# Kernel optimization log

Hardware: AMD Instinct MI355X
Metric: run time of the kernel (lower is better)

The kernel has to match this reference:

```python
import jax, jax.numpy as jnp
import numpy as np

P = 512       # protein_dim
D = 512       # drug_dim
N = 2000      # neighbors per layer
E = 300000    # binding edges per layer
ND = 100000   # total drugs
BASELINE = 6.0
LN_EPS = 1e-5


def setup_inputs() -> dict:
    key = jax.random.key(0)
    ks = jax.random.split(key, 24)
    inp = {
        "target_features": jax.random.normal(ks[0], (P,), jnp.float32),
        "form_features": jax.random.normal(ks[1], (N, P), jnp.float32),
        "role_features": jax.random.normal(ks[2], (N, P), jnp.float32),
        "form_neighbors": jnp.arange(N, dtype=jnp.int64) if jax.config.jax_enable_x64 else jnp.arange(N, dtype=jnp.int32),
        "role_neighbors": jnp.arange(N, dtype=jnp.int32),
        "form_binds_ei": jax.random.randint(ks[3], (2, E), 0, N, jnp.int32),
        "form_binds_y": jax.random.uniform(ks[4], (E,), jnp.float32) * 8.0 + 2.0,
        "role_binds_ei": jax.random.randint(ks[5], (2, E), 0, N, jnp.int32),
        "role_binds_y": jax.random.uniform(ks[6], (E,), jnp.float32) * 8.0 + 2.0,
        "drug_features": jax.random.normal(ks[7], (ND, D), jnp.float32),
    }
    inp["form_neighbors"] = jnp.arange(N, dtype=jnp.int32)
    attn_in = P * 2 + 16
    s1 = 1.0 / np.sqrt(attn_in)
    s2 = 1.0 / np.sqrt(64)
    sd = 1.0 / np.sqrt(D)
    sp = 1.0 / np.sqrt(P)
    inp["layer_emb"] = jax.random.normal(ks[8], (2, 16), jnp.float32)
    inp["W1"] = jax.random.uniform(ks[9], (attn_in, 64), jnp.float32, -s1, s1)
    inp["b1"] = jax.random.uniform(ks[10], (64,), jnp.float32, -s1, s1)
    inp["W2"] = jax.random.uniform(ks[11], (64, 1), jnp.float32, -s2, s2)
    inp["b2"] = jax.random.uniform(ks[12], (1,), jnp.float32, -s2, s2)
    inp["Wi1"] = jax.random.uniform(ks[13], (D, P), jnp.float32, -sd, sd)
    inp["bi1"] = jax.random.uniform(ks[14], (P,), jnp.float32, -sd, sd)
    inp["prelu_alpha"] = jnp.array(0.25, jnp.float32)
    inp["Wi2"] = jax.random.uniform(ks[15], (P, P), jnp.float32, -sp, sp)
    inp["bi2"] = jax.random.uniform(ks[16], (P,), jnp.float32, -sp, sp)
    inp["ln_gamma"] = jnp.ones((P,), jnp.float32)
    inp["ln_beta"] = jnp.zeros((P,), jnp.float32)
    return inp


def _pref_vectors(neighbor_ids, ei, y, drug_features):
    # Vectorized form of the per-neighbor masked gather-sum:
    # for each edge, find its neighbor slot (neighbor_ids is sorted);
    # edges whose src id is not a neighbor get zero weight.
    n = neighbor_ids.shape[0]
    pos = jnp.clip(jnp.searchsorted(neighbor_ids, ei[0]), 0, n - 1)
    valid = neighbor_ids[pos] == ei[0]
    w = jnp.where(valid, y - BASELINE, 0.0)              # [E]
    contrib = drug_features[ei[1]] * w[:, None]          # [E, D] gather (memory-bound)
    return jax.ops.segment_sum(contrib, pos, num_segments=n)  # [N, D]


def _attention(z_target, z_neighbors, l_vec, W1, b1, W2, b2):
    n = z_neighbors.shape[0]
    inp = jnp.concatenate(
        [jnp.broadcast_to(z_target, (n, z_target.shape[0])),
         z_neighbors,
         jnp.broadcast_to(l_vec, (n, l_vec.shape[0]))], axis=-1)  # [N, 2P+16]
    h = inp @ W1 + b1
    h = jnp.where(h > 0, h, 0.2 * h)  # LeakyReLU(0.2)
    return h @ W2 + b2                # [N, 1]


def reference(target_features, form_features, role_features, form_neighbors,
              role_neighbors, form_binds_ei, form_binds_y, role_binds_ei,
              role_binds_y, drug_features, layer_emb, W1, b1, W2, b2,
              Wi1, bi1, prelu_alpha, Wi2, bi2, ln_gamma, ln_beta):
    form_msgs = _pref_vectors(form_neighbors, form_binds_ei, form_binds_y, drug_features)
    role_msgs = _pref_vectors(role_neighbors, role_binds_ei, role_binds_y, drug_features)

    form_attn = _attention(target_features, form_features, layer_emb[0], W1, b1, W2, b2)
    role_attn = _attention(target_features, role_features, layer_emb[1], W1, b1, W2, b2)

    all_msgs = jnp.concatenate([form_msgs, role_msgs], axis=0)   # [2N, D]
    all_attn = jnp.concatenate([form_attn, role_attn], axis=0)   # [2N, 1]
    attn_weights = jax.nn.softmax(all_attn, axis=0)
    v_prior = jnp.sum(attn_weights * all_msgs, axis=0)           # [D]

    h = v_prior @ Wi1 + bi1
    h = jnp.where(h > 0, h, prelu_alpha * h)  # PReLU
    v = h @ Wi2 + bi2                          # [P]

    x = target_features + v
    mu = jnp.mean(x)
    var = jnp.mean(jnp.square(x - mu))
    z_refined = (x - mu) / jnp.sqrt(var + LN_EPS) * ln_gamma + ln_beta
    return (z_refined, form_msgs, role_msgs)
```

## Files before the change

### kernel.cpp

```cpp
#include <hip/hip_runtime.h>
#include <math.h>

static constexpr int PD = 512;
static constexpr float BASEV = 6.0f;
static constexpr int CAP = 320;

__global__ __launch_bounds__(256) void front_kernel(
    const int* __restrict__ ei_f, const float* __restrict__ y_f,
    const int* __restrict__ ei_r, const float* __restrict__ y_r,
    const int* __restrict__ nb_f, const int* __restrict__ nb_r,
    const float* __restrict__ target, const float* __restrict__ formF,
    const float* __restrict__ roleF, const float* __restrict__ lemb,
    const float* __restrict__ W1, const float* __restrict__ b1,
    const float* __restrict__ W2, const float* __restrict__ b2,
    int N, int E, int AB, int EBf,
    int* __restrict__ cnt, int2* __restrict__ bins,
    float* __restrict__ logits) {
    __shared__ int snb[2048];
    int b = blockIdx.x;
    if (b >= AB) {
        int b2 = b - AB;
        bool role = b2 >= EBf;
        const int* nb = role ? nb_r : nb_f;
        const int* ei = role ? ei_r : ei_f;
        const float* yy = role ? y_r : y_f;
        bool lds_ok = (N <= 2048);
        if (lds_ok) {
            for (int i = threadIdx.x; i < N; i += 256) snb[i] = nb[i];
            __syncthreads();
        }
        int base = (role ? b2 - EBf : b2) * 1024;
        int K = 32 - __clz(N);
        int v[4], lo[4], hi[4], e[4];
#pragma unroll
        for (int r = 0; r < 4; r++) {
            e[r] = base + threadIdx.x + r * 256;
            bool a = e[r] < E;
            v[r] = a ? ei[e[r]] : 0;
            lo[r] = 0; hi[r] = a ? N : 0;
        }
        if (lds_ok) {
            for (int it = 0; it < K; it++) {
#pragma unroll
                for (int r = 0; r < 4; r++) {
                    if (lo[r] < hi[r]) {
                        int mid = (lo[r] + hi[r]) >> 1;
                        if (snb[mid] < v[r]) lo[r] = mid + 1; else hi[r] = mid;
                    }
                }
            }
        } else {
            for (int it = 0; it < K; it++) {
#pragma unroll
                for (int r = 0; r < 4; r++) {
                    if (lo[r] < hi[r]) {
                        int mid = (lo[r] + hi[r]) >> 1;
                        if (nb[mid] < v[r]) lo[r] = mid + 1; else hi[r] = mid;
                    }
                }
            }
        }
#pragma unroll
        for (int r = 0; r < 4; r++) {
            if (e[r] >= E) continue;
            int pos = lo[r] < N ? lo[r] : N - 1;
            int nbp = lds_ok ? snb[pos] : nb[pos];
            if (nbp != v[r]) continue;
            int s = role ? N + pos : pos;
            float w = yy[e[r]] - BASEV;
            int slot = atomicAdd(&cnt[s], 1);
            if (slot < CAP) bins[(size_t)s * CAP + slot] = make_int2(ei[E + e[r]], __float_as_int(w));
        }
    } else {
        float* spart = (float*)snb;
        float* sc0 = spart + 256;
        float* sc1 = spart + 320;
        int jj = threadIdx.x & 63, ck = threadIdx.x >> 6;
        const float* Wc = W1 + jj;
        float tp = 0.f;
        int p0 = ck * 128;
        for (int p = p0; p < p0 + 128; p += 4) {
            float4 tv = *(const float4*)(target + p);
            tp += tv.x * Wc[(size_t)(p + 0) * 64] + tv.y * Wc[(size_t)(p + 1) * 64]
                + tv.z * Wc[(size_t)(p + 2) * 64] + tv.w * Wc[(size_t)(p + 3) * 64];
        }
        spart[ck * 64 + jj] = tp;
        __syncthreads();
        if (ck == 0) {
            float c = b1[jj] + spart[jj] + spart[64 + jj] + spart[128 + jj] + spart[192 + jj];
            float c0 = c, c1 = c;
            for (int q = 0; q < 16; q++) {
                float wq = Wc[(size_t)(2 * PD + q) * 64];
                c0 += lemb[q] * wq;
                c1 += lemb[16 + q] * wq;
            }
            sc0[jj] = c0; sc1[jj] = c1;
        }
        __syncthreads();
        int wave = threadIdx.x >> 6, lane = threadIdx.x & 63;
        int rr = b * 4 + wave;
        int nseg = 2 * N;
        if (rr >= nseg) return;
        bool rl = rr >= N;
        const float* z = rl ? roleF + (size_t)(rr - N) * PD : formF + (size_t)rr * PD;
        const float* Wz = W1 + (size_t)PD * 64 + lane;
        float hA = rl ? sc1[lane] : sc0[lane];
        float hB = 0.f, hC = 0.f, hD = 0.f;
        for (int p = 0; p < PD; p += 8) {
            float4 z0 = *(const float4*)(z + p);
            float4 z1 = *(const float4*)(z + p + 4);
            hA += z0.x * Wz[(size_t)(p + 0) * 64] + z0.y * Wz[(size_t)(p + 1) * 64];
            hB += z0.z * Wz[(size_t)(p + 2) * 64] + z0.w * Wz[(size_t)(p + 3) * 64];
            hC += z1.x * Wz[(size_t)(p + 4) * 64] + z1.y * Wz[(size_t)(p + 5) * 64];
            hD += z1.z * Wz[(size_t)(p + 6) * 64] + z1.w * Wz[(size_t)(p + 7) * 64];
        }
        float hh = (hA + hB) + (hC + hD);
        hh = hh > 0.f ? hh : 0.2f * hh;
        float vv = hh * W2[lane];
#pragma unroll
        for (int off = 32; off > 0; off >>= 1) vv += __shfl_down(vv, off, 64);
        if (lane == 0) logits[rr] = vv + b2[0];
    }
}

__global__ __launch_bounds__(128) void accum_kernel(const int* __restrict__ cnt,
                                                    const int2* __restrict__ bins,
                                                    const float* __restrict__ drug,
                                                    float* __restrict__ msgs) {
    int b = blockIdx.x;
    int t = threadIdx.x;
    int n = cnt[b]; n = n < CAP ? n : CAP;
    const int2* bb = bins + (size_t)b * CAP;
    float4 acc = make_float4(0.f, 0.f, 0.f, 0.f);
    int k = 0;
    for (; k + 7 < n; k += 8) {
        int2 e0 = bb[k + 0], e1 = bb[k + 1], e2 = bb[k + 2], e3 = bb[k + 3];
        int2 e4 = bb[k + 4], e5 = bb[k + 5], e6 = bb[k + 6], e7 = bb[k + 7];
        float4 d0 = ((const float4*)(drug + (size_t)e0.x * PD))[t];
        float4 d1 = ((const float4*)(drug + (size_t)e1.x * PD))[t];
        float4 d2 = ((const float4*)(drug + (size_t)e2.x * PD))[t];
        float4 d3 = ((const float4*)(drug + (size_t)e3.x * PD))[t];
        float4 d4 = ((const float4*)(drug + (size_t)e4.x * PD))[t];
        float4 d5 = ((const float4*)(drug + (size_t)e5.x * PD))[t];
        float4 d6 = ((const float4*)(drug + (size_t)e6.x * PD))[t];
        float4 d7 = ((const float4*)(drug + (size_t)e7.x * PD))[t];
        float w0 = __int_as_float(e0.y), w1 = __int_as_float(e1.y);
        float w2 = __int_as_float(e2.y), w3 = __int_as_float(e3.y);
        float w4 = __int_as_float(e4.y), w5 = __int_as_float(e5.y);
        float w6 = __int_as_float(e6.y), w7 = __int_as_float(e7.y);
        acc.x += w0 * d0.x; acc.y += w0 * d0.y; acc.z += w0 * d0.z; acc.w += w0 * d0.w;
        acc.x += w1 * d1.x; acc.y += w1 * d1.y; acc.z += w1 * d1.z; acc.w += w1 * d1.w;
        acc.x += w2 * d2.x; acc.y += w2 * d2.y; acc.z += w2 * d2.z; acc.w += w2 * d2.w;
        acc.x += w3 * d3.x; acc.y += w3 * d3.y; acc.z += w3 * d3.z; acc.w += w3 * d3.w;
        acc.x += w4 * d4.x; acc.y += w4 * d4.y; acc.z += w4 * d4.z; acc.w += w4 * d4.w;
        acc.x += w5 * d5.x; acc.y += w5 * d5.y; acc.z += w5 * d5.z; acc.w += w5 * d5.w;
        acc.x += w6 * d6.x; acc.y += w6 * d6.y; acc.z += w6 * d6.z; acc.w += w6 * d6.w;
        acc.x += w7 * d7.x; acc.y += w7 * d7.y; acc.z += w7 * d7.z; acc.w += w7 * d7.w;
    }
    for (; k < n; k++) {
        int2 e0 = bb[k];
        float w0 = __int_as_float(e0.y);
        float4 d0 = ((const float4*)(drug + (size_t)e0.x * PD))[t];
        acc.x += w0 * d0.x; acc.y += w0 * d0.y; acc.z += w0 * d0.z; acc.w += w0 * d0.w;
    }
    ((float4*)(msgs + (size_t)b * PD))[t] = acc;
}

__global__ __launch_bounds__(128) void vprior_kernel(const float* __restrict__ logits,
                                                     const float* __restrict__ msgs,
                                                     int nseg, float* __restrict__ v_prior) {
    __shared__ float red[128];
    int t = threadIdx.x;
    float m = -1e30f;
    for (int s = t; s < nseg; s += 128) m = fmaxf(m, logits[s]);
    red[t] = m; __syncthreads();
    for (int o = 64; o > 0; o >>= 1) { if (t < o) red[t] = fmaxf(red[t], red[t + o]); __syncthreads(); }
    m = red[0]; __syncthreads();
    float sum = 0.f;
    for (int s = t; s < nseg; s += 128) sum += expf(logits[s] - m);
    red[t] = sum; __syncthreads();
    for (int o = 64; o > 0; o >>= 1) { if (t < o) red[t] += red[t + o]; __syncthreads(); }
    float inv = 1.f / red[0];

    float4 acc = make_float4(0.f, 0.f, 0.f, 0.f);
    for (int s = blockIdx.x; s < nseg; s += gridDim.x) {
        float w = expf(logits[s] - m) * inv;
        float4 d = ((const float4*)(msgs + (size_t)s * PD))[t];
        acc.x += w * d.x; acc.y += w * d.y; acc.z += w * d.z; acc.w += w * d.w;
    }
    atomicAdd(&v_prior[4 * t + 0], acc.x);
    atomicAdd(&v_prior[4 * t + 1], acc.y);
    atomicAdd(&v_prior[4 * t + 2], acc.z);
    atomicAdd(&v_prior[4 * t + 3], acc.w);
}

__global__ __launch_bounds__(256) void mv1_kernel(const float* __restrict__ v_prior,
                                                  const float* __restrict__ Wi1,
                                                  float* __restrict__ h) {
    int b = blockIdx.x;
    int t = threadIdx.x;
    float2 acc = make_float2(0.f, 0.f);
    int d0 = b * 16;
    for (int d = d0; d < d0 + 16; d++) {
        float vd = v_prior[d];
        float2 w = ((const float2*)(Wi1 + (size_t)d * PD))[t];
        acc.x += vd * w.x; acc.y += vd * w.y;
    }
    atomicAdd(&h[2 * t + 0], acc.x);
    atomicAdd(&h[2 * t + 1], acc.y);
}

__global__ __launch_bounds__(256) void mv2_kernel(const float* __restrict__ h,
                                                  const float* __restrict__ bi1,
                                                  const float* __restrict__ alpha_p,
                                                  const float* __restrict__ Wi2,
                                                  float* __restrict__ v) {
    int b = blockIdx.x;
    int t = threadIdx.x;
    float alpha = alpha_p[0];
    float2 acc = make_float2(0.f, 0.f);
    int q0 = b * 16;
    for (int q = q0; q < q0 + 16; q++) {
        float hq = h[q] + bi1[q];
        hq = hq > 0.f ? hq : alpha * hq;
        float2 w = ((const float2*)(Wi2 + (size_t)q * PD))[t];
        acc.x += hq * w.x; acc.y += hq * w.y;
    }
    atomicAdd(&v[2 * t + 0], acc.x);
    atomicAdd(&v[2 * t + 1], acc.y);
}

__global__ __launch_bounds__(512) void final_kernel(const float* __restrict__ target,
                                                    const float* __restrict__ v,
                                                    const float* __restrict__ bi2,
                                                    const float* __restrict__ gamma,
                                                    const float* __restrict__ beta,
                                                    float* __restrict__ out) {
    __shared__ float red[512];
    int t = threadIdx.x;
    float x = target[t] + v[t] + bi2[t];
    red[t] = x; __syncthreads();
    for (int o = 256; o > 0; o >>= 1) { if (t < o) red[t] += red[t + o]; __syncthreads(); }
    float mu = red[0] * (1.f / 512.f);
    __syncthreads();
    float dx = x - mu;
    red[t] = dx * dx; __syncthreads();
    for (int o = 256; o > 0; o >>= 1) { if (t < o) red[t] += red[t + o]; __syncthreads(); }
    float var = red[0] * (1.f / 512.f);
    out[t] = dx * (1.f / sqrtf(var + 1e-5f)) * gamma[t] + beta[t];
}

extern "C" void kernel_launch(void* const* d_in, const int* in_sizes, int n_in,
                              void* d_out, int out_size, void* d_ws, size_t ws_size,
                              hipStream_t stream) {
    const float* target = (const float*)d_in[0];
    const float* formF  = (const float*)d_in[1];
    const float* roleF  = (const float*)d_in[2];
    const int*   nb_f   = (const int*)d_in[3];
    const int*   nb_r   = (const int*)d_in[4];
    const int*   ei_f   = (const int*)d_in[5];
    const float* y_f    = (const float*)d_in[6];
    const int*   ei_r   = (const int*)d_in[7];
    const float* y_r    = (const float*)d_in[8];
    const float* drug   = (const float*)d_in[9];
    const float* lemb   = (const float*)d_in[10];
    const float* W1     = (const float*)d_in[11];
    const float* b1     = (const float*)d_in[12];
    const float* W2     = (const float*)d_in[13];
    const float* b2     = (const float*)d_in[14];
    const float* Wi1    = (const float*)d_in[15];
    const float* bi1    = (const float*)d_in[16];
    const float* alpha  = (const float*)d_in[17];
    const float* Wi2    = (const float*)d_in[18];
    const float* bi2    = (const float*)d_in[19];
    const float* gamma  = (const float*)d_in[20];
    const float* beta   = (const float*)d_in[21];

    int N = in_sizes[3];
    int E = in_sizes[5] / 2;
    int nseg = 2 * N;

    int* ws = (int*)d_ws;
    int*   cnt     = ws + 0;
    float* v_prior = (float*)(ws + 4096);
    float* hbuf    = (float*)(ws + 4608);
    float* vbuf    = (float*)(ws + 5120);
    float* logits  = (float*)(ws + 5632);
    int2*  bins    = (int2*)(ws + 9728);

    float* out  = (float*)d_out;
    float* msgs = out + PD;

    hipMemsetAsync(ws, 0, 5632 * sizeof(int), stream);

    int AB  = (nseg + 3) / 4;
    int EBf = (E + 1023) / 1024;
    front_kernel<<<AB + 2 * EBf, 256, 0, stream>>>(ei_f, y_f, ei_r, y_r, nb_f, nb_r,
                                                   target, formF, roleF, lemb,
                                                   W1, b1, W2, b2, N, E, AB, EBf,
                                                   cnt, bins, logits);
    accum_kernel<<<nseg, 128, 0, stream>>>(cnt, bins, drug, msgs);
    vprior_kernel<<<64, 128, 0, stream>>>(logits, msgs, nseg, v_prior);
    mv1_kernel<<<32, 256, 0, stream>>>(v_prior, Wi1, hbuf);
    mv2_kernel<<<32, 256, 0, stream>>>(hbuf, bi1, alpha, Wi2, vbuf);
    final_kernel<<<1, 512, 0, stream>>>(target, vbuf, bi2, gamma, beta, out);
}
```

Baseline: 452.8 us.

## Use direct-index neighbor lookup, move softmax stats into accum, nontemporal bins

Result: faster. 443.3 us (-2.1%).

```diff
diff --git a/kernel.cpp b/kernel.cpp
--- a/kernel.cpp
+++ b/kernel.cpp
@@ -4,6 +4,10 @@
 static constexpr int PD = 512;
 static constexpr float BASEV = 6.0f;
 static constexpr int CAP = 320;
+
+typedef float f4v __attribute__((ext_vector_type(4)));
+typedef int   i4v __attribute__((ext_vector_type(4)));
+typedef int   i2v __attribute__((ext_vector_type(2)));
 
 __global__ __launch_bounds__(256) void front_kernel(
     const int* __restrict__ ei_f, const float* __restrict__ y_f,
@@ -16,7 +20,7 @@
     int N, int E, int AB, int EBf,
     int* __restrict__ cnt, int2* __restrict__ bins,
     float* __restrict__ logits) {
-    __shared__ int snb[2048];
+    __shared__ float sred[384];
     int b = blockIdx.x;
     if (b >= AB) {
         int b2 = b - AB;
@@ -24,55 +28,33 @@
         const int* nb = role ? nb_r : nb_f;
         const int* ei = role ? ei_r : ei_f;
         const float* yy = role ? y_r : y_f;
-        bool lds_ok = (N <= 2048);
-        if (lds_ok) {
-            for (int i = threadIdx.x; i < N; i += 256) snb[i] = nb[i];
-            __syncthreads();
-        }
         int base = (role ? b2 - EBf : b2) * 1024;
-        int K = 32 - __clz(N);
-        int v[4], lo[4], hi[4], e[4];
+        int nb0 = nb[0];
 #pragma unroll
         for (int r = 0; r < 4; r++) {
-            e[r] = base + threadIdx.x + r * 256;
-            bool a = e[r] < E;
-            v[r] = a ? ei[e[r]] : 0;
-            lo[r] = 0; hi[r] = a ? N : 0;
-        }
-        if (lds_ok) {
-            for (int it = 0; it < K; it++) {
-#pragma unroll
-                for (int r = 0; r < 4; r++) {
-                    if (lo[r] < hi[r]) {
-                        int mid = (lo[r] + hi[r]) >> 1;
-                        if (snb[mid] < v[r]) lo[r] = mid + 1; else hi[r] = mid;
-                    }
-                }
+            int e = base + threadIdx.x + r * 256;
+            if (e >= E) continue;
+            int v = ei[e];
+            int g = v - nb0; g = g < 0 ? 0 : (g >= N ? N - 1 : g);
+            int pos;
+            if (nb[g] == v && (g == 0 || nb[g - 1] < v)) {
+                pos = g;
+            } else {
+                int lo = 0, hi = N;
+                while (lo < hi) { int mid = (lo + hi) >> 1; if (nb[mid] < v) lo = mid + 1; else hi = mid; }
+                pos = lo < N ? lo : N - 1;
+                if (nb[pos] != v) continue;
             }
-        } else {
-            for (int it = 0; it < K; it++) {
-#pragma unroll
-                for (int r = 0; r < 4; r++) {
-                    if (lo[r] < hi[r]) {
-                        int mid = (lo[r] + hi[r]) >> 1;
-                        if (nb[mid] < v[r]) lo[r] = mid + 1; else hi[r] = mid;
-                    }
-                }
+            int s = role ? N + pos : pos;
+            float w = yy[e] - BASEV;
+            int slot = atomicAdd(&cnt[s], 1);
+            if (slot < CAP) {
+                i2v val; val.x = ei[E + e]; val.y = __float_as_int(w);
+                __builtin_nontemporal_store(val, reinterpret_cast<i2v*>(bins + (size_t)s * CAP + slot));
             }
         }
-#pragma unroll
-        for (int r = 0; r < 4; r++) {
-            if (e[r] >= E) continue;
-            int pos = lo[r] < N ? lo[r] : N - 1;
-            int nbp = lds_ok ? snb[pos] : nb[pos];
-            if (nbp != v[r]) continue;
-            int s = role ? N + pos : pos;
-            float w = yy[e[r]] - BASEV;
-            int slot = atomicAdd(&cnt[s], 1);
-            if (slot < CAP) bins[(size_t)s * CAP + slot] = make_int2(ei[E + e[r]], __float_as_int(w));
-        }
     } else {
-        float* spart = (float*)snb;
+        float* spart = sred;
         float* sc0 = spart + 256;
         float* sc1 = spart + 320;
         int jj = threadIdx.x & 63, ck = threadIdx.x >> 6;
@@ -126,28 +108,47 @@
 __global__ __launch_bounds__(128) void accum_kernel(const int* __restrict__ cnt,
                                                     const int2* __restrict__ bins,
                                                     const float* __restrict__ drug,
+                                                    const float* __restrict__ logits,
+                                                    int nseg,
+                                                    float* __restrict__ sm,
                                                     float* __restrict__ msgs) {
     int b = blockIdx.x;
     int t = threadIdx.x;
+    if (b == nseg) {
+        __shared__ float red[128];
+        float m = -1e30f;
+        for (int s = t; s < nseg; s += 128) m = fmaxf(m, logits[s]);
+        red[t] = m; __syncthreads();
+        for (int o = 64; o > 0; o >>= 1) { if (t < o) red[t] = fmaxf(red[t], red[t + o]); __syncthreads(); }
+        m = red[0]; __syncthreads();
+        float sum = 0.f;
+        for (int s = t; s < nseg; s += 128) sum += expf(logits[s] - m);
+        red[t] = sum; __syncthreads();
+        for (int o = 64; o > 0; o >>= 1) { if (t < o) red[t] += red[t + o]; __syncthreads(); }
+        if (t == 0) { sm[0] = m; sm[1] = red[0]; }
+        return;
+    }
     int n = cnt[b]; n = n < CAP ? n : CAP;
     const int2* bb = bins + (size_t)b * CAP;
     float4 acc = make_float4(0.f, 0.f, 0.f, 0.f);
     int k = 0;
     for (; k + 7 < n; k += 8) {
-        int2 e0 = bb[k + 0], e1 = bb[k + 1], e2 = bb[k + 2], e3 = bb[k + 3];
-        int2 e4 = bb[k + 4], e5 = bb[k + 5], e6 = bb[k + 6], e7 = bb[k + 7];
-        float4 d0 = ((const float4*)(drug + (size_t)e0.x * PD))[t];
-        float4 d1 = ((const float4*)(drug + (size_t)e1.x * PD))[t];
-        float4 d2 = ((const float4*)(drug + (size_t)e2.x * PD))[t];
-        float4 d3 = ((const float4*)(drug + (size_t)e3.x * PD))[t];
-        float4 d4 = ((const float4*)(drug + (size_t)e4.x * PD))[t];
-        float4 d5 = ((const float4*)(drug + (size_t)e5.x * PD))[t];
-        float4 d6 = ((const float4*)(drug + (size_t)e6.x * PD))[t];
-        float4 d7 = ((const float4*)(drug + (size_t)e7.x * PD))[t];
-        float w0 = __int_as_float(e0.y), w1 = __int_as_float(e1.y);
-        float w2 = __int_as_float(e2.y), w3 = __int_as_float(e3.y);
-        float w4 = __int_as_float(e4.y), w5 = __int_as_float(e5.y);
-        float w6 = __int_as_float(e6.y), w7 = __int_as_float(e7.y);
+        i4v q0 = __builtin_nontemporal_load(reinterpret_cast<const i4v*>(bb + k + 0));
+        i4v q1 = __builtin_nontemporal_load(reinterpret_cast<const i4v*>(bb + k + 2));
+        i4v q2 = __builtin_nontemporal_load(reinterpret_cast<const i4v*>(bb + k + 4));
+        i4v q3 = __builtin_nontemporal_load(reinterpret_cast<const i4v*>(bb + k + 6));
+        float4 d0 = ((const float4*)(drug + (size_t)q0.x * PD))[t];
+        float4 d1 = ((const float4*)(drug + (size_t)q0.z * PD))[t];
+        float4 d2 = ((const float4*)(drug + (size_t)q1.x * PD))[t];
+        float4 d3 = ((const float4*)(drug + (size_t)q1.z * PD))[t];
+        float4 d4 = ((const float4*)(drug + (size_t)q2.x * PD))[t];
+        float4 d5 = ((const float4*)(drug + (size_t)q2.z * PD))[t];
+        float4 d6 = ((const float4*)(drug + (size_t)q3.x * PD))[t];
+        float4 d7 = ((const float4*)(drug + (size_t)q3.z * PD))[t];
+        float w0 = __int_as_float(q0.y), w1 = __int_as_float(q0.w);
+        float w2 = __int_as_float(q1.y), w3 = __int_as_float(q1.w);
+        float w4 = __int_as_float(q2.y), w5 = __int_as_float(q2.w);
+        float w6 = __int_as_float(q3.y), w7 = __int_as_float(q3.w);
         acc.x += w0 * d0.x; acc.y += w0 * d0.y; acc.z += w0 * d0.z; acc.w += w0 * d0.w;
         acc.x += w1 * d1.x; acc.y += w1 * d1.y; acc.z += w1 * d1.z; acc.w += w1 * d1.w;
         acc.x += w2 * d2.x; acc.y += w2 * d2.y; acc.z += w2 * d2.z; acc.w += w2 * d2.w;
@@ -163,25 +164,17 @@
         float4 d0 = ((const float4*)(drug + (size_t)e0.x * PD))[t];
         acc.x += w0 * d0.x; acc.y += w0 * d0.y; acc.z += w0 * d0.z; acc.w += w0 * d0.w;
     }
-    ((float4*)(msgs + (size_t)b * PD))[t] = acc;
+    f4v av; av.x = acc.x; av.y = acc.y; av.z = acc.z; av.w = acc.w;
+    __builtin_nontemporal_store(av, reinterpret_cast<f4v*>(msgs + (size_t)b * PD) + t);
 }
 
 __global__ __launch_bounds__(128) void vprior_kernel(const float* __restrict__ logits,
                                                      const float* __restrict__ msgs,
+                                                     const float* __restrict__ sm,
                                                      int nseg, float* __restrict__ v_prior) {
-    __shared__ float red[128];
-    int t = threadIdx.x;
-    float m = -1e30f;
-    for (int s = t; s < nseg; s += 128) m = fmaxf(m, logits[s]);
-    red[t] = m; __syncthreads();
-    for (int o = 64; o > 0; o >>= 1) { if (t < o) red[t] = fmaxf(red[t], red[t + o]); __syncthreads(); }
-    m = red[0]; __syncthreads();
-    float sum = 0.f;
-    for (int s = t; s < nseg; s += 128) sum += expf(logits[s] - m);
-    red[t] = sum; __syncthreads();
-    for (int o = 64; o > 0; o >>= 1) { if (t < o) red[t] += red[t + o]; __syncthreads(); }
-    float inv = 1.f / red[0];
-
+    int t = threadIdx.x;
+    float m = sm[0];
+    float inv = 1.f / sm[1];
     float4 acc = make_float4(0.f, 0.f, 0.f, 0.f);
     for (int s = blockIdx.x; s < nseg; s += gridDim.x) {
         float w = expf(logits[s] - m) * inv;
@@ -286,7 +279,8 @@
     float* hbuf    = (float*)(ws + 4608);
     float* vbuf    = (float*)(ws + 5120);
     float* logits  = (float*)(ws + 5632);
-    int2*  bins    = (int2*)(ws + 9728);
+    float* smbuf   = (float*)(ws + 9728);
+    int2*  bins    = (int2*)(ws + 9730 + 6);
 
     float* out  = (float*)d_out;
     float* msgs = out + PD;
@@ -299,8 +293,8 @@
                                                    target, formF, roleF, lemb,
                                                    W1, b1, W2, b2, N, E, AB, EBf,
                                                    cnt, bins, logits);
-    accum_kernel<<<nseg, 128, 0, stream>>>(cnt, bins, drug, msgs);
-    vprior_kernel<<<64, 128, 0, stream>>>(logits, msgs, nseg, v_prior);
+    accum_kernel<<<nseg + 1, 128, 0, stream>>>(cnt, bins, drug, logits, nseg, smbuf, msgs);
+    vprior_kernel<<<256, 128, 0, stream>>>(logits, msgs, smbuf, nseg, v_prior);
     mv1_kernel<<<32, 256, 0, stream>>>(v_prior, Wi1, hbuf);
     mv2_kernel<<<32, 256, 0, stream>>>(hbuf, bi1, alpha, Wi2, vbuf);
     final_kernel<<<1, 512, 0, stream>>>(target, vbuf, bi2, gamma, beta, out);
```
